# Optimization experiments

Measured on AMD Instinct MI355X. Metric: run time of the kernel, lower is better.

## Reference

```python
import jax, jax.numpy as jnp
import numpy as np

D_MODEL = 1024
NUM_HEADS = 16
HEAD_DIM = D_MODEL // NUM_HEADS  # 64
THETA = 10000.0
B, S = 2, 2048


def setup_inputs() -> dict:
    key = jax.random.key(0)
    k1, k2, k3 = jax.random.split(key, 3)
    sigma_qkv = (2.0 / (D_MODEL + 3 * D_MODEL)) ** 0.5
    sigma_o = (2.0 / (D_MODEL + D_MODEL)) ** 0.5
    x = jax.random.normal(k1, (B, S, D_MODEL), dtype=jnp.float32)
    w_qkv = jax.random.normal(k2, (3 * D_MODEL, D_MODEL), dtype=jnp.float32) * sigma_qkv
    w_o = jax.random.normal(k3, (D_MODEL, D_MODEL), dtype=jnp.float32) * sigma_o
    token_positions = jnp.arange(S, dtype=jnp.int32)
    return {"x": x, "w_qkv": w_qkv, "w_o": w_o, "token_positions": token_positions, "mask": 1}


def _rope(t, pos):
    # t: (B, H, S, HEAD_DIM); pos: (S,) int
    ids = jnp.arange(HEAD_DIM // 2, dtype=jnp.float32)
    freqs = pos.astype(jnp.float32)[:, None] * (THETA ** (-2.0 * ids / HEAD_DIM))  # (S, HEAD_DIM/2)
    cos, sin = jnp.cos(freqs), jnp.sin(freqs)
    even, odd = t[..., 0::2], t[..., 1::2]
    r_even = even * cos - odd * sin
    r_odd = odd * cos + even * sin
    # interleave back to original layout
    return jnp.stack([r_even, r_odd], axis=-1).reshape(t.shape)


def reference(x, w_qkv, w_o, token_positions, mask):
    # fused QKV projection: Linear computes x @ W^T with W [out, in]
    qkv = x @ w_qkv.T  # (B, S, 3*D_MODEL)
    q, k, v = jnp.split(qkv, 3, axis=-1)

    def to_heads(t):
        return t.reshape(B, S, NUM_HEADS, HEAD_DIM).transpose(0, 2, 1, 3)  # (B, H, S, Dh)

    q, k, v = to_heads(q), to_heads(k), to_heads(v)
    q = _rope(q, token_positions)
    k = _rope(k, token_positions)

    scores = jnp.einsum('bhqd,bhkd->bhqk', q, k)
    if mask:  # causal: lower-triangular allowed
        causal = jnp.tril(jnp.ones((S, S), dtype=bool))
        scores = jnp.where(causal, scores, -jnp.inf)
    attn = jax.nn.softmax(scores * (HEAD_DIM ** -0.5), axis=-1)
    out = jnp.einsum('bhqk,bhkd->bhqd', attn, v)  # (B, H, S, Dh)
    out = out.transpose(0, 2, 1, 3).reshape(B, S, D_MODEL)
    return out @ w_o.T
```

## Files before the change

kernel.cpp:

```cpp
#include <hip/hip_runtime.h>
#include <hip/hip_bf16.h>
#include <math.h>

typedef __bf16 bf16_t;
typedef __bf16 bf16x8 __attribute__((ext_vector_type(8)));
typedef __bf16 bf16x4 __attribute__((ext_vector_type(4)));
typedef float  f32x4  __attribute__((ext_vector_type(4)));
typedef float  f32x16 __attribute__((ext_vector_type(16)));

#define D_MODEL 1024
#define NH      16
#define HD      64
#define BATCH   2
#define SEQ     2048
#define MROWS   (BATCH*SEQ)
#define QKVN    (3*D_MODEL)
#define FA_PAD  72
#define SCALE_LOG2E 0.18033688011112042f

__device__ __forceinline__ void async_cp16(const bf16_t* g, bf16_t* l) {
    __builtin_amdgcn_global_load_lds(
        (const __attribute__((address_space(1))) void*)g,
        (__attribute__((address_space(3))) void*)l,
        16, 0, 0);
}

__device__ __forceinline__ float fexp2(float x) {
    float r;
    asm("v_exp_f32 %0, %1" : "=v"(r) : "v"(x));
    return r;
}

__device__ __forceinline__ unsigned cvtpk(float lo, float hi_) {
    unsigned r;
    asm("v_cvt_pk_bf16_f32 %0, %1, %2" : "=v"(r) : "v"(lo), "v"(hi_));
    return r;
}

__global__ void cvt_all(const float* __restrict__ x, const float* __restrict__ wq,
                        const float* __restrict__ wo,
                        bf16_t* __restrict__ xb, bf16_t* __restrict__ wqb,
                        bf16_t* __restrict__ wob) {
    const int nx = MROWS * D_MODEL, nq = QKVN * D_MODEL;
    int i = (blockIdx.x * blockDim.x + threadIdx.x) * 4;
    const float* s; bf16_t* d; int off;
    if (i < nx)           { s = x;  d = xb;  off = i; }
    else if (i < nx + nq) { s = wq; d = wqb; off = i - nx; }
    else                  { s = wo; d = wob; off = i - nx - nq; }
    float4 v = *(const float4*)(s + off);
    d[off]     = (bf16_t)v.x;
    d[off + 1] = (bf16_t)v.y;
    d[off + 2] = (bf16_t)v.z;
    d[off + 3] = (bf16_t)v.w;
}

template <typename OutT, int NI>
__global__ __launch_bounds__(256) void gemm_nt(const bf16_t* __restrict__ A,
                                               const bf16_t* __restrict__ Bm,
                                               OutT* __restrict__ C,
                                               int M, int N, int K) {
    __shared__ __align__(16) bf16_t AsA[128 * 32], AsB[128 * 32];
    __shared__ __align__(16) bf16_t BsA[NI * 32 * 32], BsB[NI * 32 * 32];
    const int tid  = threadIdx.x;
    const int w    = tid >> 6;
    const int lane = tid & 63;
    const int quad = lane >> 4;
    const int l16  = lane & 15;
    const int m0   = blockIdx.x * 128;
    const int n0   = blockIdx.y * (NI * 32);
    const int wm   = (w >> 1) * 64;
    const int wn   = (w & 1) * (NI * 16);

    f32x4 acc[4][NI];
    #pragma unroll
    for (int i = 0; i < 4; i++)
        #pragma unroll
        for (int j = 0; j < NI; j++)
            acc[i][j] = (f32x4){0.f, 0.f, 0.f, 0.f};

    const bf16_t* Ag0 = A  + (size_t)(m0 + (tid >> 2)) * K + (tid & 3) * 8;
    const bf16_t* Ag1 = Ag0 + (size_t)64 * K;
    const bf16_t* Bg0 = Bm + (size_t)(n0 + (tid >> 2)) * K + (tid & 3) * 8;
    const bf16_t* Bg1 = Bg0 + (size_t)64 * K;

    for (int k0 = 0; k0 < K; k0 += 64) {
        async_cp16(Ag0 + k0,      &AsA[(size_t)tid * 8]);
        async_cp16(Ag1 + k0,      &AsA[((size_t)tid + 256) * 8]);
        async_cp16(Ag0 + k0 + 32, &AsB[(size_t)tid * 8]);
        async_cp16(Ag1 + k0 + 32, &AsB[((size_t)tid + 256) * 8]);
        async_cp16(Bg0 + k0,      &BsA[(size_t)tid * 8]);
        async_cp16(Bg0 + k0 + 32, &BsB[(size_t)tid * 8]);
        if (NI == 4) {
            async_cp16(Bg1 + k0,      &BsA[((size_t)tid + 256) * 8]);
            async_cp16(Bg1 + k0 + 32, &BsB[((size_t)tid + 256) * 8]);
        }
        __syncthreads();

        bf16x8 af[4][2], bfr[NI][2];
        #pragma unroll
        for (int mi = 0; mi < 4; mi++) {
            af[mi][0] = *(const bf16x8*)&AsA[(wm + mi * 16 + l16) * 32 + quad * 8];
            af[mi][1] = *(const bf16x8*)&AsB[(wm + mi * 16 + l16) * 32 + quad * 8];
        }
        #pragma unroll
        for (int ni = 0; ni < NI; ni++) {
            bfr[ni][0] = *(const bf16x8*)&BsA[(wn + ni * 16 + l16) * 32 + quad * 8];
            bfr[ni][1] = *(const bf16x8*)&BsB[(wn + ni * 16 + l16) * 32 + quad * 8];
        }
        #pragma unroll
        for (int mi = 0; mi < 4; mi++)
            #pragma unroll
            for (int ni = 0; ni < NI; ni++) {
                acc[mi][ni] = __builtin_amdgcn_mfma_f32_16x16x32_bf16(
                    af[mi][0], bfr[ni][0], acc[mi][ni], 0, 0, 0);
                acc[mi][ni] = __builtin_amdgcn_mfma_f32_16x16x32_bf16(
                    af[mi][1], bfr[ni][1], acc[mi][ni], 0, 0, 0);
            }
        __syncthreads();
    }

    #pragma unroll
    for (int mi = 0; mi < 4; mi++)
        #pragma unroll
        for (int ni = 0; ni < NI; ni++) {
            const int col = n0 + wn + ni * 16 + l16;
            #pragma unroll
            for (int r = 0; r < 4; r++) {
                const int row = m0 + wm + mi * 16 + quad * 4 + r;
                C[(size_t)row * N + col] = (OutT)acc[mi][ni][r];
            }
        }
}

__global__ __launch_bounds__(256) void rope_split(const bf16_t* __restrict__ qkv,
                                                  const int* __restrict__ pos,
                                                  bf16_t* __restrict__ Qh,
                                                  bf16_t* __restrict__ Kh,
                                                  bf16_t* __restrict__ VT) {
    __shared__ bf16_t vs[128][FA_PAD];
    const int tid   = threadIdx.x;
    const int s_loc = tid >> 1;
    const int half  = tid & 1;
    const int s0    = blockIdx.x * 128;
    const int bh    = blockIdx.y;
    const int b     = bh >> 4, h = bh & 15;
    const int s     = s0 + s_loc;

    const bf16_t* row = qkv + (size_t)(b * SEQ + s) * QKVN + h * HD + half * 32;

    bf16_t qbuf[32], kbuf[32], vbuf[32];
    #pragma unroll
    for (int j = 0; j < 4; j++) {
        *(bf16x8*)&qbuf[j * 8] = *(const bf16x8*)(row + j * 8);
        *(bf16x8*)&kbuf[j * 8] = *(const bf16x8*)(row + D_MODEL + j * 8);
        *(bf16x8*)&vbuf[j * 8] = *(const bf16x8*)(row + 2 * D_MODEL + j * 8);
    }

    const float pf = (float)pos[s];
    #pragma unroll
    for (int p = 0; p < 16; p++) {
        const int d2 = half * 16 + p;
        const float inv = __expf(-0.28782313662425575f * (float)d2);
        const float f = pf * inv;
        const float c = __cosf(f), sn = __sinf(f);
        float qe = (float)qbuf[2 * p], qo = (float)qbuf[2 * p + 1];
        float ke = (float)kbuf[2 * p], ko = (float)kbuf[2 * p + 1];
        qbuf[2 * p]     = (bf16_t)((qe * c - qo * sn) * SCALE_LOG2E);
        qbuf[2 * p + 1] = (bf16_t)((qo * c + qe * sn) * SCALE_LOG2E);
        kbuf[2 * p]     = (bf16_t)(ke * c - ko * sn);
        kbuf[2 * p + 1] = (bf16_t)(ko * c + ke * sn);
    }

    bf16_t* qdst = Qh + ((size_t)bh * SEQ + s) * HD + half * 32;
    bf16_t* kdst = Kh + ((size_t)bh * SEQ + s) * HD + half * 32;
    #pragma unroll
    for (int j = 0; j < 4; j++) {
        *(bf16x8*)(qdst + j * 8) = *(bf16x8*)&qbuf[j * 8];
        *(bf16x8*)(kdst + j * 8) = *(bf16x8*)&kbuf[j * 8];
        *(bf16x8*)&vs[s_loc][half * 32 + j * 8] = *(bf16x8*)&vbuf[j * 8];
    }
    __syncthreads();

    const int d  = tid >> 2;
    const int sc = tid & 3;
    bf16_t tmp[32];
    #pragma unroll
    for (int i = 0; i < 32; i++) tmp[i] = vs[sc * 32 + i][d];
    bf16_t* vdst = VT + ((size_t)bh * HD + d) * SEQ + s0 + sc * 32;
    #pragma unroll
    for (int j = 0; j < 4; j++)
        *(bf16x8*)(vdst + j * 8) = *(bf16x8*)&tmp[j * 8];
}

__global__ __launch_bounds__(256) void flash_attn(const bf16_t* __restrict__ Qh,
                                                  const bf16_t* __restrict__ Kh,
                                                  const bf16_t* __restrict__ VT,
                                                  bf16_t* __restrict__ AO) {
    __shared__ __align__(16) bf16_t smem[4 * 64 * FA_PAD];
    bf16_t* Ks0 = smem;
    bf16_t* Vs0 = smem + 2 * 64 * FA_PAD;
    const int BUF = 64 * FA_PAD;

    const int tid  = threadIdx.x;
    const int w    = tid >> 6;
    const int lane = tid & 63;
    const int l31  = lane & 31;
    const int hi   = lane >> 5;
    const int qh   = w & 1;
    const int kh   = w >> 1;

    const int bid  = blockIdx.x;
    const int bh   = bid & 31;
    const int my_t = 31 - (bid >> 5);
    const int nkv  = my_t + 1;

    const bf16_t* Qb = Qh + (size_t)bh * SEQ * HD;
    const bf16_t* Kb = Kh + (size_t)bh * SEQ * HD;
    const bf16_t* Vb = VT + (size_t)bh * HD * SEQ;

    const int q0b = my_t * 64;
    const int qlo = q0b + qh * 32;
    const int qg  = qlo + l31;

    bf16x8 aq[4];
    #pragma unroll
    for (int ks = 0; ks < 4; ks++)
        aq[ks] = *(const bf16x8*)(Qb + (size_t)qg * HD + ks * 16 + hi * 8);

    const int srow = tid >> 3, scol = (tid & 7) * 8;
    const int lds0 = srow * FA_PAD + scol;
    const int lds1 = (srow + 32) * FA_PAD + scol;

    f32x16 o[2];
    #pragma unroll
    for (int dt = 0; dt < 2; dt++)
        #pragma unroll
        for (int i = 0; i < 16; i++) o[dt][i] = 0.f;
    float ls = 0.f;

    bf16x8 pK0 = *(const bf16x8*)(Kb + (size_t)srow * HD + scol);
    bf16x8 pK1 = *(const bf16x8*)(Kb + (size_t)(srow + 32) * HD + scol);
    bf16x8 pV0 = *(const bf16x8*)(Vb + (size_t)srow * SEQ + scol);
    bf16x8 pV1 = *(const bf16x8*)(Vb + (size_t)(srow + 32) * SEQ + scol);
    *(bf16x8*)&Ks0[lds0] = pK0;
    *(bf16x8*)&Ks0[lds1] = pK1;
    *(bf16x8*)&Vs0[lds0] = pV0;
    *(bf16x8*)&Vs0[lds1] = pV1;

    for (int kt = 0; kt < nkv; ++kt) {
        const int cur = kt & 1;
        __syncthreads();

        if (kt + 1 < nkv) {
            const int kn = (kt + 1) * 64;
            pK0 = *(const bf16x8*)(Kb + (size_t)(kn + srow) * HD + scol);
            pK1 = *(const bf16x8*)(Kb + (size_t)(kn + srow + 32) * HD + scol);
            pV0 = *(const bf16x8*)(Vb + (size_t)srow * SEQ + kn + scol);
            pV1 = *(const bf16x8*)(Vb + (size_t)(srow + 32) * SEQ + kn + scol);
        }

        const bf16_t* KsC = Ks0 + cur * BUF;
        const bf16_t* VsC = Vs0 + cur * BUF;
        const int kvbw = kt * 64 + kh * 32;
        if (kvbw <= qlo + 31) {
            const bool full = (kvbw + 31 <= qlo);

            bf16x8 kb[4];
            #pragma unroll
            for (int ks = 0; ks < 4; ks++)
                kb[ks] = *(const bf16x8*)&KsC[(kh * 32 + l31) * FA_PAD + ks * 16 + hi * 8];
            f32x16 t;
            #pragma unroll
            for (int i = 0; i < 16; i++) t[i] = 0.f;
            #pragma unroll
            for (int ks = 0; ks < 4; ks++)
                t = __builtin_amdgcn_mfma_f32_32x32x16_bf16(kb[ks], aq[ks], t, 0, 0, 0);

            float pv[16];
            #pragma unroll
            for (int r = 0; r < 16; r++) {
                float p = fexp2(t[r]);
                if (!full) {
                    const int kvg = kvbw + (r & 3) + 8 * (r >> 2) + 4 * hi;
                    if (kvg > qg) p = 0.f;
                }
                pv[r] = p;
            }
            ls += ((((pv[0] + pv[1]) + (pv[2] + pv[3]))
                  + ((pv[4] + pv[5]) + (pv[6] + pv[7])))
                 + (((pv[8] + pv[9]) + (pv[10] + pv[11]))
                  + ((pv[12] + pv[13]) + (pv[14] + pv[15]))));

            union { unsigned u[4]; bf16x8 v; } pa0, pa1;
            {
                unsigned a0 = cvtpk(pv[0], pv[1]);
                unsigned b0 = cvtpk(pv[4], pv[5]);
                unsigned a1 = cvtpk(pv[2], pv[3]);
                unsigned b1 = cvtpk(pv[6], pv[7]);
                asm volatile("v_permlane32_swap_b32 %0, %1" : "+v"(a0), "+v"(b0));
                asm volatile("v_permlane32_swap_b32 %0, %1" : "+v"(a1), "+v"(b1));
                pa0.u[0] = a0; pa0.u[1] = a1; pa0.u[2] = b0; pa0.u[3] = b1;
            }
            {
                unsigned a0 = cvtpk(pv[8], pv[9]);
                unsigned b0 = cvtpk(pv[12], pv[13]);
                unsigned a1 = cvtpk(pv[10], pv[11]);
                unsigned b1 = cvtpk(pv[14], pv[15]);
                asm volatile("v_permlane32_swap_b32 %0, %1" : "+v"(a0), "+v"(b0));
                asm volatile("v_permlane32_swap_b32 %0, %1" : "+v"(a1), "+v"(b1));
                pa1.u[0] = a0; pa1.u[1] = a1; pa1.u[2] = b0; pa1.u[3] = b1;
            }

            #pragma unroll
            for (int dt = 0; dt < 2; dt++) {
                const int vbase = (dt * 32 + l31) * FA_PAD + kh * 32 + hi * 8;
                bf16x8 vf0 = *(const bf16x8*)&VsC[vbase];
                bf16x8 vf1 = *(const bf16x8*)&VsC[vbase + 16];
                o[dt] = __builtin_amdgcn_mfma_f32_32x32x16_bf16(pa0.v, vf0, o[dt], 0, 0, 0);
                o[dt] = __builtin_amdgcn_mfma_f32_32x32x16_bf16(pa1.v, vf1, o[dt], 0, 0, 0);
            }
        }

        if (kt + 1 < nkv) {
            bf16_t* KsN = Ks0 + (cur ^ 1) * BUF;
            bf16_t* VsN = Vs0 + (cur ^ 1) * BUF;
            *(bf16x8*)&KsN[lds0] = pK0;
            *(bf16x8*)&KsN[lds1] = pK1;
            *(bf16x8*)&VsN[lds0] = pV0;
            *(bf16x8*)&VsN[lds1] = pV1;
        }
    }

    __syncthreads();
    ls += __shfl_xor(ls, 32);
    float* mrgO = (float*)smem;
    float* lsp  = mrgO + 2 * 32 * 66;
    if (kh == 1) {
        #pragma unroll
        for (int r = 0; r < 16; r++) {
            const int qlc = (r & 3) + 8 * (r >> 2) + 4 * hi;
            #pragma unroll
            for (int dt = 0; dt < 2; dt++)
                mrgO[(qh * 32 + qlc) * 66 + dt * 32 + l31] = o[dt][r];
        }
        if (hi == 0) lsp[qh * 32 + l31] = ls;
    }
    __syncthreads();
    if (kh == 0) {
        const float lt = ls + lsp[qh * 32 + l31];
        const int b = bh >> 4, hh = bh & 15;
        #pragma unroll
        for (int r = 0; r < 16; r++) {
            const int qlc = (r & 3) + 8 * (r >> 2) + 4 * hi;
            const float li = 1.0f / __shfl(lt, qlc);
            const size_t row = (size_t)b * SEQ + q0b + qh * 32 + qlc;
            #pragma unroll
            for (int dt = 0; dt < 2; dt++) {
                const float v = o[dt][r] + mrgO[(qh * 32 + qlc) * 66 + dt * 32 + l31];
                AO[row * D_MODEL + hh * HD + dt * 32 + l31] = (bf16_t)(v * li);
            }
        }
    }
}

extern "C" void kernel_launch(void* const* d_in, const int* in_sizes, int n_in,
                              void* d_out, int out_size, void* d_ws, size_t ws_size,
                              hipStream_t stream) {
    const float* x     = (const float*)d_in[0];
    const float* w_qkv = (const float*)d_in[1];
    const float* w_o   = (const float*)d_in[2];
    const int*   tpos  = (const int*)d_in[3];
    float*       out   = (float*)d_out;

    char* ws = (char*)d_ws;
    bf16_t* xb  = (bf16_t*)(ws);
    bf16_t* wqb = (bf16_t*)(ws + 8388608);
    bf16_t* wob = (bf16_t*)(ws + 14680064);
    bf16_t* qkv = (bf16_t*)(ws + 16777216);
    bf16_t* Qh  = (bf16_t*)(ws + 41943040);
    bf16_t* Kh  = (bf16_t*)(ws + 50331648);
    bf16_t* VT  = (bf16_t*)(ws + 58720256);
    bf16_t* AO  = (bf16_t*)(ws + 67108864);

    cvt_all<<<8192, 256, 0, stream>>>(x, w_qkv, w_o, xb, wqb, wob);

    gemm_nt<bf16_t, 4><<<dim3(32, 24), 256, 0, stream>>>(xb, wqb, qkv, MROWS, QKVN, D_MODEL);

    rope_split<<<dim3(SEQ / 128, BATCH * NH), 256, 0, stream>>>(qkv, tpos, Qh, Kh, VT);

    flash_attn<<<1024, 256, 0, stream>>>(Qh, Kh, VT, AO);

    gemm_nt<float, 2><<<dim3(32, 16), 256, 0, stream>>>(AO, wob, out, MROWS, D_MODEL, D_MODEL);
}
```

Measured before the change: 185.6 us.

## Load K/V fragments directly from global into registers, dropping LDS staging

The flash attention loop no longer stages K and V tiles in double-buffered shared memory with per-iteration barriers. Each wave now loads its K fragments straight from global memory into registers, one tile ahead using two ping-ponged register sets, and loads its V fragments from global inside each step. Shared memory is shrunk to just the final cross-wave merge buffer. This removes the __syncthreads and LDS traffic but duplicates global/L2 reads across waves that share a tile, and the V loads are no longer prefetched, so their latency is exposed.

```diff
diff --git a/kernel.cpp b/kernel.cpp
--- a/kernel.cpp
+++ b/kernel.cpp
@@ -196,10 +196,7 @@
                                                   const bf16_t* __restrict__ Kh,
                                                   const bf16_t* __restrict__ VT,
                                                   bf16_t* __restrict__ AO) {
-    __shared__ __align__(16) bf16_t smem[4 * 64 * FA_PAD];
-    bf16_t* Ks0 = smem;
-    bf16_t* Vs0 = smem + 2 * 64 * FA_PAD;
-    const int BUF = 64 * FA_PAD;
+    __shared__ __align__(16) float mrg[2 * 32 * 66 + 64];
 
     const int tid  = threadIdx.x;
     const int w    = tid >> 6;
@@ -227,10 +224,6 @@
     for (int ks = 0; ks < 4; ks++)
         aq[ks] = *(const bf16x8*)(Qb + (size_t)qg * HD + ks * 16 + hi * 8);
 
-    const int srow = tid >> 3, scol = (tid & 7) * 8;
-    const int lds0 = srow * FA_PAD + scol;
-    const int lds1 = (srow + 32) * FA_PAD + scol;
-
     f32x16 o[2];
     #pragma unroll
     for (int dt = 0; dt < 2; dt++)
@@ -238,103 +231,90 @@
         for (int i = 0; i < 16; i++) o[dt][i] = 0.f;
     float ls = 0.f;
 
-    bf16x8 pK0 = *(const bf16x8*)(Kb + (size_t)srow * HD + scol);
-    bf16x8 pK1 = *(const bf16x8*)(Kb + (size_t)(srow + 32) * HD + scol);
-    bf16x8 pV0 = *(const bf16x8*)(Vb + (size_t)srow * SEQ + scol);
-    bf16x8 pV1 = *(const bf16x8*)(Vb + (size_t)(srow + 32) * SEQ + scol);
-    *(bf16x8*)&Ks0[lds0] = pK0;
-    *(bf16x8*)&Ks0[lds1] = pK1;
-    *(bf16x8*)&Vs0[lds0] = pV0;
-    *(bf16x8*)&Vs0[lds1] = pV1;
-
-    for (int kt = 0; kt < nkv; ++kt) {
-        const int cur = kt & 1;
-        __syncthreads();
-
-        if (kt + 1 < nkv) {
-            const int kn = (kt + 1) * 64;
-            pK0 = *(const bf16x8*)(Kb + (size_t)(kn + srow) * HD + scol);
-            pK1 = *(const bf16x8*)(Kb + (size_t)(kn + srow + 32) * HD + scol);
-            pV0 = *(const bf16x8*)(Vb + (size_t)srow * SEQ + kn + scol);
-            pV1 = *(const bf16x8*)(Vb + (size_t)(srow + 32) * SEQ + kn + scol);
-        }
-
-        const bf16_t* KsC = Ks0 + cur * BUF;
-        const bf16_t* VsC = Vs0 + cur * BUF;
-        const int kvbw = kt * 64 + kh * 32;
-        if (kvbw <= qlo + 31) {
-            const bool full = (kvbw + 31 <= qlo);
-
-            bf16x8 kb[4];
-            #pragma unroll
-            for (int ks = 0; ks < 4; ks++)
-                kb[ks] = *(const bf16x8*)&KsC[(kh * 32 + l31) * FA_PAD + ks * 16 + hi * 8];
-            f32x16 t;
-            #pragma unroll
-            for (int i = 0; i < 16; i++) t[i] = 0.f;
-            #pragma unroll
-            for (int ks = 0; ks < 4; ks++)
-                t = __builtin_amdgcn_mfma_f32_32x32x16_bf16(kb[ks], aq[ks], t, 0, 0, 0);
-
-            float pv[16];
-            #pragma unroll
-            for (int r = 0; r < 16; r++) {
-                float p = fexp2(t[r]);
-                if (!full) {
-                    const int kvg = kvbw + (r & 3) + 8 * (r >> 2) + 4 * hi;
-                    if (kvg > qg) p = 0.f;
-                }
-                pv[r] = p;
-            }
-            ls += ((((pv[0] + pv[1]) + (pv[2] + pv[3]))
-                  + ((pv[4] + pv[5]) + (pv[6] + pv[7])))
-                 + (((pv[8] + pv[9]) + (pv[10] + pv[11]))
-                  + ((pv[12] + pv[13]) + (pv[14] + pv[15]))));
-
-            union { unsigned u[4]; bf16x8 v; } pa0, pa1;
-            {
-                unsigned a0 = cvtpk(pv[0], pv[1]);
-                unsigned b0 = cvtpk(pv[4], pv[5]);
-                unsigned a1 = cvtpk(pv[2], pv[3]);
-                unsigned b1 = cvtpk(pv[6], pv[7]);
-                asm volatile("v_permlane32_swap_b32 %0, %1" : "+v"(a0), "+v"(b0));
-                asm volatile("v_permlane32_swap_b32 %0, %1" : "+v"(a1), "+v"(b1));
-                pa0.u[0] = a0; pa0.u[1] = a1; pa0.u[2] = b0; pa0.u[3] = b1;
-            }
-            {
-                unsigned a0 = cvtpk(pv[8], pv[9]);
-                unsigned b0 = cvtpk(pv[12], pv[13]);
-                unsigned a1 = cvtpk(pv[10], pv[11]);
-                unsigned b1 = cvtpk(pv[14], pv[15]);
-                asm volatile("v_permlane32_swap_b32 %0, %1" : "+v"(a0), "+v"(b0));
-                asm volatile("v_permlane32_swap_b32 %0, %1" : "+v"(a1), "+v"(b1));
-                pa1.u[0] = a0; pa1.u[1] = a1; pa1.u[2] = b0; pa1.u[3] = b1;
-            }
-
-            #pragma unroll
-            for (int dt = 0; dt < 2; dt++) {
-                const int vbase = (dt * 32 + l31) * FA_PAD + kh * 32 + hi * 8;
-                bf16x8 vf0 = *(const bf16x8*)&VsC[vbase];
-                bf16x8 vf1 = *(const bf16x8*)&VsC[vbase + 16];
-                o[dt] = __builtin_amdgcn_mfma_f32_32x32x16_bf16(pa0.v, vf0, o[dt], 0, 0, 0);
-                o[dt] = __builtin_amdgcn_mfma_f32_32x32x16_bf16(pa1.v, vf1, o[dt], 0, 0, 0);
-            }
-        }
-
-        if (kt + 1 < nkv) {
-            bf16_t* KsN = Ks0 + (cur ^ 1) * BUF;
-            bf16_t* VsN = Vs0 + (cur ^ 1) * BUF;
-            *(bf16x8*)&KsN[lds0] = pK0;
-            *(bf16x8*)&KsN[lds1] = pK1;
-            *(bf16x8*)&VsN[lds0] = pV0;
-            *(bf16x8*)&VsN[lds1] = pV1;
-        }
-    }
+#define LOADK(KB, CC) do {                                                     \
+    const int _cl = (CC) < nkv ? (CC) : nkv - 1;                               \
+    const bf16_t* _kp = Kb + (size_t)(_cl * 64 + kh * 32 + l31) * HD + hi * 8; \
+    KB[0] = *(const bf16x8*)_kp;                                               \
+    KB[1] = *(const bf16x8*)(_kp + 16);                                        \
+    KB[2] = *(const bf16x8*)(_kp + 32);                                        \
+    KB[3] = *(const bf16x8*)(_kp + 48);                                        \
+} while (0)
+
+#define STEP(KB, CC) do {                                                      \
+    const int kvbw = (CC) * 64 + kh * 32;                                      \
+    if ((CC) < nkv && kvbw <= qlo + 31) {                                      \
+        const bool full = (kvbw + 31 <= qlo);                                  \
+        bf16x8 vf[2][2];                                                       \
+        _Pragma("unroll")                                                      \
+        for (int dt = 0; dt < 2; dt++) {                                       \
+            const bf16_t* _vp = Vb + (size_t)(dt * 32 + l31) * SEQ + kvbw + hi * 8; \
+            vf[dt][0] = *(const bf16x8*)_vp;                                   \
+            vf[dt][1] = *(const bf16x8*)(_vp + 16);                            \
+        }                                                                      \
+        f32x16 t;                                                              \
+        _Pragma("unroll")                                                      \
+        for (int i = 0; i < 16; i++) t[i] = 0.f;                               \
+        _Pragma("unroll")                                                      \
+        for (int ks = 0; ks < 4; ks++)                                         \
+            t = __builtin_amdgcn_mfma_f32_32x32x16_bf16(KB[ks], aq[ks], t, 0, 0, 0); \
+        float pv[16];                                                          \
+        _Pragma("unroll")                                                      \
+        for (int r = 0; r < 16; r++) {                                         \
+            float p = fexp2(t[r]);                                             \
+            if (!full) {                                                       \
+                const int kvg = kvbw + (r & 3) + 8 * (r >> 2) + 4 * hi;        \
+                if (kvg > qg) p = 0.f;                                         \
+            }                                                                  \
+            pv[r] = p;                                                         \
+        }                                                                      \
+        ls += ((((pv[0] + pv[1]) + (pv[2] + pv[3]))                            \
+              + ((pv[4] + pv[5]) + (pv[6] + pv[7])))                           \
+             + (((pv[8] + pv[9]) + (pv[10] + pv[11]))                          \
+              + ((pv[12] + pv[13]) + (pv[14] + pv[15]))));                     \
+        union { unsigned u[4]; bf16x8 v; } pa0, pa1;                           \
+        {                                                                      \
+            unsigned a0 = cvtpk(pv[0], pv[1]);                                 \
+            unsigned b0 = cvtpk(pv[4], pv[5]);                                 \
+            unsigned a1 = cvtpk(pv[2], pv[3]);                                 \
+            unsigned b1 = cvtpk(pv[6], pv[7]);                                 \
+            asm volatile("v_permlane32_swap_b32 %0, %1" : "+v"(a0), "+v"(b0)); \
+            asm volatile("v_permlane32_swap_b32 %0, %1" : "+v"(a1), "+v"(b1)); \
+            pa0.u[0] = a0; pa0.u[1] = a1; pa0.u[2] = b0; pa0.u[3] = b1;        \
+        }                                                                      \
+        {                                                                      \
+            unsigned a0 = cvtpk(pv[8], pv[9]);                                 \
+            unsigned b0 = cvtpk(pv[12], pv[13]);                               \
+            unsigned a1 = cvtpk(pv[10], pv[11]);                               \
+            unsigned b1 = cvtpk(pv[14], pv[15]);                               \
+            asm volatile("v_permlane32_swap_b32 %0, %1" : "+v"(a0), "+v"(b0)); \
+            asm volatile("v_permlane32_swap_b32 %0, %1" : "+v"(a1), "+v"(b1)); \
+            pa1.u[0] = a0; pa1.u[1] = a1; pa1.u[2] = b0; pa1.u[3] = b1;        \
+        }                                                                      \
+        _Pragma("unroll")                                                      \
+        for (int dt = 0; dt < 2; dt++) {                                       \
+            o[dt] = __builtin_amdgcn_mfma_f32_32x32x16_bf16(pa0.v, vf[dt][0], o[dt], 0, 0, 0); \
+            o[dt] = __builtin_amdgcn_mfma_f32_32x32x16_bf16(pa1.v, vf[dt][1], o[dt], 0, 0, 0); \
+        }                                                                      \
+    }                                                                          \
+} while (0)
+
+    bf16x8 kA[4], kB[4];
+    LOADK(kA, 0);
+    for (int c2 = 0; c2 < nkv; c2 += 2) {
+        LOADK(kB, c2 + 1);
+        STEP(kA, c2);
+        if (c2 + 1 < nkv) {
+            LOADK(kA, c2 + 2);
+            STEP(kB, c2 + 1);
+        }
+    }
+#undef LOADK
+#undef STEP
 
     __syncthreads();
     ls += __shfl_xor(ls, 32);
-    float* mrgO = (float*)smem;
-    float* lsp  = mrgO + 2 * 32 * 66;
+    float* mrgO = mrg;
+    float* lsp  = mrg + 2 * 32 * 66;
     if (kh == 1) {
         #pragma unroll
         for (int r = 0; r < 16; r++) {
```

Measured after the change: 216.7 us. 1.17x slower.
